# Optimization experiments

Hardware: AMD Instinct MI355X
Metric: run time of the kernel (lower is better)

The kernel has to match this reference:

```python
import jax, jax.numpy as jnp
import numpy as np

T, B, Y, H, R, L = 256, 1024, 32, 1024, 512, 2  # seq_len, batch, y_dim, h_dim, rnn_dim, n_layers


def setup_inputs() -> dict:
    key = jax.random.key(0)
    ks = jax.random.split(key, 18)
    s = jnp.float32(0.05)

    def w(k, shape):
        return jax.random.normal(k, shape, dtype=jnp.float32) * s

    return {
        "y": jax.random.normal(ks[0], (T, B, Y), dtype=jnp.float32),
        # decoder MLP: Linear(R->H), ReLU, Linear(H->H), ReLU
        "dec_w1": w(ks[1], (H, R)), "dec_b1": jnp.zeros((H,), jnp.float32),
        "dec_w2": w(ks[2], (H, H)), "dec_b2": jnp.zeros((H,), jnp.float32),
        # dec_mean: Linear(H->Y); dec_std: Linear(H->Y) + Softplus
        "mean_w": w(ks[3], (Y, H)), "mean_b": jnp.zeros((Y,), jnp.float32),
        "std_w": w(ks[4], (Y, H)), "std_b": jnp.zeros((Y,), jnp.float32),
        # 2-layer GRU, torch gate order (r, z, n)
        "gru_wih0": w(ks[5], (3 * R, Y)), "gru_whh0": w(ks[6], (3 * R, R)),
        "gru_bih0": jnp.zeros((3 * R,), jnp.float32), "gru_bhh0": jnp.zeros((3 * R,), jnp.float32),
        "gru_wih1": w(ks[7], (3 * R, R)), "gru_whh1": w(ks[8], (3 * R, R)),
        "gru_bih1": jnp.zeros((3 * R,), jnp.float32), "gru_bhh1": jnp.zeros((3 * R,), jnp.float32),
    }


def _gru_cell(x, h, wih, whh, bih, bhh):
    # torch GRUCell math, gates ordered (r, z, n)
    gi = x @ wih.T + bih          # [B, 3R]
    gh = h @ whh.T + bhh          # [B, 3R]
    ir, iz, inn = jnp.split(gi, 3, axis=-1)
    hr, hz, hn = jnp.split(gh, 3, axis=-1)
    r = jax.nn.sigmoid(ir + hr)
    z = jax.nn.sigmoid(iz + hz)
    n = jnp.tanh(inn + r * hn)
    return (1.0 - z) * n + z * h


def reference(y, dec_w1, dec_b1, dec_w2, dec_b2, mean_w, mean_b, std_w, std_b,
              gru_wih0, gru_whh0, gru_bih0, gru_bhh0,
              gru_wih1, gru_whh1, gru_bih1, gru_bhh1):
    log2pi = jnp.float32(np.log(2.0 * np.pi))
    batch = y.shape[1]
    h0 = jnp.zeros((L, batch, R), dtype=y.dtype)

    def step(carry, y_t):
        h, nll = carry
        # decode from top-layer hidden state (before the GRU update)
        d = jax.nn.relu(h[-1] @ dec_w1.T + dec_b1)
        d = jax.nn.relu(d @ dec_w2.T + dec_b2)
        mean_t = d @ mean_w.T + mean_b
        std_t = jax.nn.softplus(d @ std_w.T + std_b)
        # nll_gauss: 0.5 * sum((x-mu)^2/std^2 + 2*log(std) + log(2*pi))
        nll_t = 0.5 * jnp.sum((y_t - mean_t) ** 2 / (std_t ** 2)
                              + 2.0 * jnp.log(std_t) + log2pi)
        # single GRU step (2 layers)
        h_l0 = _gru_cell(y_t, h[0], gru_wih0, gru_whh0, gru_bih0, gru_bhh0)
        h_l1 = _gru_cell(h_l0, h[1], gru_wih1, gru_whh1, gru_bih1, gru_bhh1)
        return (jnp.stack([h_l0, h_l1]), nll + nll_t), None

    (_, nll), _ = jax.lax.scan(step, (h0, jnp.float32(0.0)), y)
    return nll
```

## Files before the change

kernel.cpp:

```cpp
#include <hip/hip_runtime.h>
#include <math.h>

#define TT   256
#define BB   1024
#define YDIM 32
#define HDIM 1024
#define RDIM 512

typedef __attribute__((ext_vector_type(8))) short frag8;
typedef __attribute__((ext_vector_type(4))) float f32x4;

#define LDS_BUF 16384

#define OFF_NLL   ((size_t)0)
#define OFF_HAF   ((size_t)4096)
#define SZ_HF     ((size_t)BB*RDIM*4)
#define OFF_HBF   (OFF_HAF + 2*SZ_HF)
#define OFF_HA16  (OFF_HBF + 2*SZ_HF)
#define SZ_H16    ((size_t)BB*RDIM*2)
#define OFF_HB16  (OFF_HA16 + 2*SZ_H16)
#define OFF_D1    (OFF_HB16 + 2*SZ_H16)
#define SZ_DBUF   ((size_t)BB*HDIM*2)
#define OFF_D2    (OFF_D1 + 2*SZ_DBUF)
#define OFF_Y16   (OFF_D2 + 2*SZ_DBUF)
#define OFF_WG0I  (OFF_Y16 + (size_t)TT*BB*YDIM*2)
#define OFF_WG0H  (OFF_WG0I + (size_t)1536*YDIM*2)
#define OFF_WG1I  (OFF_WG0H + (size_t)1536*RDIM*2)
#define OFF_WG1H  (OFF_WG1I + (size_t)1536*RDIM*2)
#define OFF_WD1   (OFF_WG1H + (size_t)1536*RDIM*2)
#define OFF_WD2   (OFF_WD1 + (size_t)HDIM*RDIM*2)
#define OFF_WMS   (OFF_WD2 + (size_t)HDIM*HDIM*2)
#define OFF_BI0   (OFF_WMS + (size_t)64*HDIM*2)
#define OFF_BH0   (OFF_BI0 + 1536*4)
#define OFF_BI1   (OFF_BH0 + 1536*4)
#define OFF_BH1   (OFF_BI1 + 1536*4)

__device__ __forceinline__ short f2bf(float f) {
  union { float f; unsigned u; } v; v.f = f;
  unsigned r = (v.u + 0x7fffu + ((v.u >> 16) & 1u)) >> 16;
  return (short)r;
}
__device__ __forceinline__ void cvt8(const float* s, short* d) {
  float4 a = *(const float4*)s;
  float4 b = *(const float4*)(s + 4);
  frag8 v;
  v[0]=f2bf(a.x); v[1]=f2bf(a.y); v[2]=f2bf(a.z); v[3]=f2bf(a.w);
  v[4]=f2bf(b.x); v[5]=f2bf(b.y); v[6]=f2bf(b.z); v[7]=f2bf(b.w);
  *(frag8*)d = v;
}
__device__ __forceinline__ int permRow(int n) {
  int q = n / 48, r = n - 48 * q, g = r >> 4, u = r & 15;
  return g * 512 + q * 16 + u;
}
__device__ __forceinline__ float sigf(float x) { return 1.0f / (1.0f + expf(-x)); }

__device__ __forceinline__ void gload16(const short* g, short* l) {
  __builtin_amdgcn_global_load_lds(
      (const __attribute__((address_space(1))) void*)g,
      (__attribute__((address_space(3))) void*)l, 16, 0, 0);
}

template<int MF, int NF>
__device__ __forceinline__ void kloop64(
    const short* __restrict__ A, int lda, int m0,
    const short* __restrict__ B, int ldb, int nrowsB, int K,
    int wm, int wn, short* lds, f32x4 (*acc)[NF], int tid)
{
  const int l = tid & 63, w = tid >> 6, u = l & 15, quad = l >> 4;
  const int nk = K >> 6;
  const int bunits = nrowsB << 3;

  auto stage = [&](int kc, int buf) {
    short* base = lds + buf * LDS_BUF;
    const int k0 = kc << 6;
    for (int c = (w << 6); c < 1024; c += 256) {
      int p = c + l, r = p >> 3, q = (p & 7) ^ (r & 7);
      gload16(A + (size_t)(m0 + r) * lda + k0 + (q << 3), base + (c << 3));
    }
    short* bb = base + 8192;
    for (int c = (w << 6); c < bunits; c += 256) {
      int p = c + l, r = p >> 3, q = (p & 7) ^ (r & 7);
      gload16(B + (size_t)r * ldb + k0 + (q << 3), bb + (c << 3));
    }
  };

  stage(0, 0);
  __syncthreads();
  for (int kc = 0; kc < nk; ++kc) {
    if (kc + 1 < nk) stage(kc + 1, (kc + 1) & 1);
    const short* base = lds + (kc & 1) * LDS_BUF;
#pragma unroll
    for (int kk2 = 0; kk2 < 2; ++kk2) {
      const int q = (kk2 << 2) + quad;
      const int aoff = (q ^ (u & 7)) << 3;
      frag8 a[MF], b[NF];
#pragma unroll
      for (int i = 0; i < MF; ++i)
        a[i] = *(const frag8*)(base + ((wm + (i << 4) + u) << 6) + aoff);
#pragma unroll
      for (int f = 0; f < NF; ++f)
        b[f] = *(const frag8*)(base + 8192 + ((wn + (f << 4) + u) << 6) + aoff);
#pragma unroll
      for (int i = 0; i < MF; ++i)
#pragma unroll
        for (int f = 0; f < NF; ++f)
          acc[i][f] = __builtin_amdgcn_mfma_f32_16x16x32_bf16(a[i], b[f], acc[i][f], 0, 0, 0);
    }
    __syncthreads();
  }
}

template<int MF, int NF>
__device__ __forceinline__ void kloop32(
    const short* __restrict__ A, int lda, int m0,
    const short* __restrict__ B, int nrowsB,
    int wm, int wn, short* lds, f32x4 (*acc)[NF], int tid)
{
  const int l = tid & 63, w = tid >> 6, u = l & 15, quad = l >> 4;
  short* base = lds;
  for (int c = (w << 6); c < 512; c += 256) {
    int p = c + l, r = p >> 2, q = (p & 3) ^ (r & 3);
    gload16(A + (size_t)(m0 + r) * lda + (q << 3), base + (c << 3));
  }
  short* bb = base + 4096;
  const int bunits = nrowsB << 2;
  for (int c = (w << 6); c < bunits; c += 256) {
    int p = c + l, r = p >> 2, q = (p & 3) ^ (r & 3);
    gload16(B + (size_t)r * 32 + (q << 3), bb + (c << 3));
  }
  __syncthreads();
  const int aoff = (quad ^ (u & 3)) << 3;
  frag8 a[MF], b[NF];
#pragma unroll
  for (int i = 0; i < MF; ++i)
    a[i] = *(const frag8*)(base + ((wm + (i << 4) + u) << 5) + aoff);
#pragma unroll
  for (int f = 0; f < NF; ++f)
    b[f] = *(const frag8*)(base + 4096 + ((wn + (f << 4) + u) << 5) + aoff);
#pragma unroll
  for (int i = 0; i < MF; ++i)
#pragma unroll
    for (int f = 0; f < NF; ++f)
      acc[i][f] = __builtin_amdgcn_mfma_f32_16x16x32_bf16(a[i], b[f], acc[i][f], 0, 0, 0);
  __syncthreads();
}

template<bool GI32>
__device__ void gru_tile(int mb, int nb,
                         const short* Ax, int ldx, const short* Wgi,
                         const short* Ah, const short* Wgh,
                         const float* bi, const float* bh,
                         const float* hold, float* hout, short* h16out,
                         short* lds, int tid)
{
  f32x4 zero = {0.f, 0.f, 0.f, 0.f};
  f32x4 gi[4][3], gh[4][3];
#pragma unroll
  for (int i = 0; i < 4; ++i)
#pragma unroll
    for (int f = 0; f < 3; ++f) { gi[i][f] = zero; gh[i][f] = zero; }
  const int w = tid >> 6, l = tid & 63, u = l & 15, quad = l >> 4;
  const int wm = (w & 1) * 64, wn = (w >> 1) * 48;
  if (GI32)
    kloop32<4, 3>(Ax, ldx, mb * 128, Wgi, 96, wm, wn, lds, gi, tid);
  else
    kloop64<4, 3>(Ax, ldx, mb * 128, Wgi, RDIM, 96, RDIM, wm, wn, lds, gi, tid);
  kloop64<4, 3>(Ah, RDIM, mb * 128, Wgh, RDIM, 96, RDIM, wm, wn, lds, gh, tid);

  const int np = nb * 96 + (w >> 1) * 48 + u;
  const float bir = bi[np], biz = bi[np + 16], bin = bi[np + 32];
  const float bhr = bh[np], bhz = bh[np + 16], bhn = bh[np + 32];
  const int unit = nb * 32 + (w >> 1) * 16 + u;
#pragma unroll
  for (int i = 0; i < 4; ++i)
#pragma unroll
    for (int j = 0; j < 4; ++j) {
      int row = mb * 128 + wm + 16 * i + quad * 4 + j;
      float r = sigf((gi[i][0][j] + bir) + (gh[i][0][j] + bhr));
      float z = sigf((gi[i][1][j] + biz) + (gh[i][1][j] + bhz));
      float n = tanhf((gi[i][2][j] + bin) + r * (gh[i][2][j] + bhn));
      float ho = hold[(size_t)row * RDIM + unit];
      float hn = (1.f - z) * n + z * ho;
      hout[(size_t)row * RDIM + unit] = hn;
      h16out[(size_t)row * RDIM + unit] = f2bf(hn);
    }
}

__device__ void dec_tile(int mb, int nb, const short* A, int lda, int K,
                         const short* W, const float* bias, short* outp,
                         short* lds, int tid)
{
  f32x4 zero = {0.f, 0.f, 0.f, 0.f};
  f32x4 acc[4][4];
#pragma unroll
  for (int i = 0; i < 4; ++i)
#pragma unroll
    for (int f = 0; f < 4; ++f) acc[i][f] = zero;
  const int w = tid >> 6, l = tid & 63, u = l & 15, quad = l >> 4;
  const int wm = (w & 1) * 64, wn = (w >> 1) * 64;
  kloop64<4, 4>(A, lda, mb * 128, W, K, 128, K, wm, wn, lds, acc, tid);
  const int colb = nb * 128 + wn + u;
  float bv[4];
#pragma unroll
  for (int f = 0; f < 4; ++f) bv[f] = bias[colb + 16 * f];
#pragma unroll
  for (int i = 0; i < 4; ++i)
#pragma unroll
    for (int f = 0; f < 4; ++f)
#pragma unroll
      for (int j = 0; j < 4; ++j) {
        int row = mb * 128 + wm + 16 * i + quad * 4 + j;
        float v = acc[i][f][j] + bv[f];
        if (v < 0.f) v = 0.f;
        outp[(size_t)row * HDIM + colb + 16 * f] = f2bf(v);
      }
}

__device__ void ms_tile(int mb, int tstep, const short* d2p, const short* Wms,
                        const float* mbias, const float* sbias, const float* y,
                        float* nll, short* lds, int tid)
{
  f32x4 zero = {0.f, 0.f, 0.f, 0.f};
  f32x4 acc[2][4];
#pragma unroll
  for (int i = 0; i < 2; ++i)
#pragma unroll
    for (int f = 0; f < 4; ++f) acc[i][f] = zero;
  const int w = tid >> 6, l = tid & 63, u = l & 15, quad = l >> 4;
  kloop64<2, 4>(d2p, HDIM, mb * 128, Wms, HDIM, 64, HDIM, w * 32, 0, lds, acc, tid);
  float lsum = 0.f;
#pragma unroll
  for (int i = 0; i < 2; ++i)
#pragma unroll
    for (int j = 0; j < 4; ++j) {
      int row = mb * 128 + w * 32 + 16 * i + quad * 4 + j;
      const float* yr = y + ((size_t)tstep * BB + row) * YDIM;
#pragma unroll
      for (int f = 0; f < 2; ++f) {
        int c = 16 * f + u;
        float m  = acc[i][f][j] + mbias[c];
        float sp = acc[i][f + 2][j] + sbias[c];
        float sg = (sp > 20.f) ? sp : log1pf(expf(sp));
        float dv = (yr[c] - m) / sg;
        lsum += dv * dv + 2.f * logf(sg) + 1.8378770664093453f;
      }
    }
  lsum *= 0.5f;
#pragma unroll
  for (int o = 32; o; o >>= 1) lsum += __shfl_xor(lsum, o);
  if (l == 0) atomicAdd(nll, lsum);
}

__global__ __launch_bounds__(256) void prepack_kernel(
    const float* y, const float* dw1, const float* dw2,
    const float* mw, const float* sw,
    const float* wih0, const float* whh0, const float* bih0, const float* bhh0,
    const float* wih1, const float* whh1, const float* bih1, const float* bhh1,
    char* __restrict__ ws)
{
  const size_t g = (size_t)blockIdx.x * 256 + threadIdx.x;
  const size_t N = (size_t)gridDim.x * 256;
  float4 z4 = {0.f, 0.f, 0.f, 0.f};
  float4* hz = (float4*)(ws + OFF_HAF);
  for (size_t i = g; i < (size_t)4 * BB * RDIM / 4; i += N) hz[i] = z4;
  int4 zi = {0, 0, 0, 0};
  int4* h16z = (int4*)(ws + OFF_HA16);
  for (size_t i = g; i < (size_t)4 * BB * RDIM / 8; i += N) h16z[i] = zi;
  if (g == 0) *(float*)(ws + OFF_NLL) = 0.f;

  short* y16  = (short*)(ws + OFF_Y16);
  short* Wg0i = (short*)(ws + OFF_WG0I);
  short* Wg0h = (short*)(ws + OFF_WG0H);
  short* Wg1i = (short*)(ws + OFF_WG1I);
  short* Wg1h = (short*)(ws + OFF_WG1H);
  short* Wd1  = (short*)(ws + OFF_WD1);
  short* Wd2  = (short*)(ws + OFF_WD2);
  short* Wms  = (short*)(ws + OFF_WMS);
  float* bi0  = (float*)(ws + OFF_BI0);
  float* bh0  = (float*)(ws + OFF_BH0);
  float* bi1  = (float*)(ws + OFF_BI1);
  float* bh1  = (float*)(ws + OFF_BH1);

  for (size_t s = g; s < (size_t)TT * BB * YDIM / 8; s += N)
    cvt8(y + s * 8, y16 + s * 8);
  for (size_t s = g; s < (size_t)1536 * RDIM / 8; s += N) {
    int row = (int)(s >> 6), seg = (int)(s & 63) << 3;
    int pr = permRow(row);
    cvt8(whh0 + (size_t)pr * RDIM + seg, Wg0h + (size_t)row * RDIM + seg);
    cvt8(wih1 + (size_t)pr * RDIM + seg, Wg1i + (size_t)row * RDIM + seg);
    cvt8(whh1 + (size_t)pr * RDIM + seg, Wg1h + (size_t)row * RDIM + seg);
  }
  for (size_t s = g; s < (size_t)1536 * YDIM / 8; s += N) {
    int row = (int)(s >> 2), seg = (int)(s & 3) << 3;
    cvt8(wih0 + (size_t)permRow(row) * YDIM + seg, Wg0i + (size_t)row * YDIM + seg);
  }
  for (size_t s = g; s < (size_t)HDIM * RDIM / 8; s += N)
    cvt8(dw1 + s * 8, Wd1 + s * 8);
  for (size_t s = g; s < (size_t)HDIM * HDIM / 8; s += N)
    cvt8(dw2 + s * 8, Wd2 + s * 8);
  for (size_t s = g; s < (size_t)64 * HDIM / 8; s += N) {
    int row = (int)(s >> 7), seg = (int)(s & 127) << 3;
    const float* src = (row < 32) ? (mw + (size_t)row * HDIM + seg)
                                  : (sw + (size_t)(row - 32) * HDIM + seg);
    cvt8(src, Wms + (size_t)row * HDIM + seg);
  }
  for (size_t s = g; s < 1536; s += N) {
    int pr = permRow((int)s);
    bi0[s] = bih0[pr]; bh0[s] = bhh0[pr];
    bi1[s] = bih1[pr]; bh1[s] = bhh1[pr];
  }
}

__global__ __launch_bounds__(256, 2) void phase_kernel(
    int p, const float* __restrict__ y,
    const float* db1, const float* db2, const float* mbias, const float* sbias,
    char* __restrict__ ws)
{
  __shared__ short lds[2 * LDS_BUF];
  const int tid = threadIdx.x;
  const int t = blockIdx.x;
  const int cur = p & 1, prv = cur ^ 1;

  float* hAf = (float*)(ws + OFF_HAF);
  float* hBf = (float*)(ws + OFF_HBF);
  short* hA16 = (short*)(ws + OFF_HA16);
  short* hB16 = (short*)(ws + OFF_HB16);
  short* d10 = (short*)(ws + OFF_D1);
  short* d20 = (short*)(ws + OFF_D2);
  const short* y16 = (const short*)(ws + OFF_Y16);

  float* hAfc = hAf + (size_t)cur * BB * RDIM;
  float* hAfp = hAf + (size_t)prv * BB * RDIM;
  float* hBfc = hBf + (size_t)cur * BB * RDIM;
  float* hBfp = hBf + (size_t)prv * BB * RDIM;
  short* hA16c = hA16 + (size_t)cur * BB * RDIM;
  short* hA16p = hA16 + (size_t)prv * BB * RDIM;
  short* hB16c = hB16 + (size_t)cur * BB * RDIM;
  short* hB16p = hB16 + (size_t)prv * BB * RDIM;
  short* d1c = d10 + (size_t)cur * BB * HDIM;
  short* d1p = d10 + (size_t)prv * BB * HDIM;
  short* d2c = d20 + (size_t)cur * BB * HDIM;
  short* d2p = d20 + (size_t)prv * BB * HDIM;

  const short* Wg0i = (const short*)(ws + OFF_WG0I);
  const short* Wg0h = (const short*)(ws + OFF_WG0H);
  const short* Wg1i = (const short*)(ws + OFF_WG1I);
  const short* Wg1h = (const short*)(ws + OFF_WG1H);
  const short* Wd1  = (const short*)(ws + OFF_WD1);
  const short* Wd2  = (const short*)(ws + OFF_WD2);
  const short* Wms  = (const short*)(ws + OFF_WMS);
  const float* bi0  = (const float*)(ws + OFF_BI0);
  const float* bh0  = (const float*)(ws + OFF_BH0);
  const float* bi1  = (const float*)(ws + OFF_BI1);
  const float* bh1  = (const float*)(ws + OFF_BH1);
  float* nllp = (float*)(ws + OFF_NLL);

  if (t < 128) {
    if (p >= 1 && p <= 255) {
      int mb = t >> 4, nb = t & 15;
      gru_tile<false>(mb, nb,
                      hA16p, RDIM, Wg1i + (size_t)nb * 96 * RDIM,
                      hB16p, Wg1h + (size_t)nb * 96 * RDIM,
                      bi1, bh1, hBfp, hBfc, hB16c, lds, tid);
    }
  } else if (t < 192) {
    if (p >= 2 && p <= 257) {
      int q = t - 128, mb = q >> 3, nb = q & 7;
      dec_tile(mb, nb, d1p, HDIM, HDIM, Wd2 + (size_t)nb * 128 * HDIM,
               db2, d2c, lds, tid);
    }
  } else if (t < 200) {
    if (p >= 3 && p <= 258) {
      ms_tile(t - 192, p - 3, d2p, Wms, mbias, sbias, y, nllp, lds, tid);
    }
  } else if (t < 328) {
    if (p <= 255) {
      int q = t - 200, mb = q >> 4, nb = q & 15;
      gru_tile<true>(mb, nb,
                     y16 + (size_t)p * BB * YDIM, YDIM, Wg0i + (size_t)nb * 96 * YDIM,
                     hA16p, Wg0h + (size_t)nb * 96 * RDIM,
                     bi0, bh0, hAfp, hAfc, hA16c, lds, tid);
    }
  } else {
    if (p >= 1 && p <= 256) {
      int q = t - 328, mb = q >> 3, nb = q & 7;
      dec_tile(mb, nb, hB16p, RDIM, RDIM, Wd1 + (size_t)nb * 128 * RDIM,
               db1, d1c, lds, tid);
    }
  }
}

__global__ void finish_kernel(float* out, const char* ws)
{
  if (threadIdx.x == 0 && blockIdx.x == 0)
    out[0] = *(const float*)(ws + OFF_NLL);
}

extern "C" void kernel_launch(void* const* d_in, const int* in_sizes, int n_in,
                              void* d_out, int out_size, void* d_ws, size_t ws_size,
                              hipStream_t stream) {
  (void)in_sizes; (void)n_in; (void)out_size; (void)ws_size;
  const float* y    = (const float*)d_in[0];
  const float* dw1  = (const float*)d_in[1];
  const float* db1  = (const float*)d_in[2];
  const float* dw2  = (const float*)d_in[3];
  const float* db2  = (const float*)d_in[4];
  const float* mw   = (const float*)d_in[5];
  const float* mbias= (const float*)d_in[6];
  const float* sw   = (const float*)d_in[7];
  const float* sbias= (const float*)d_in[8];
  const float* wih0 = (const float*)d_in[9];
  const float* whh0 = (const float*)d_in[10];
  const float* bih0 = (const float*)d_in[11];
  const float* bhh0 = (const float*)d_in[12];
  const float* wih1 = (const float*)d_in[13];
  const float* whh1 = (const float*)d_in[14];
  const float* bih1 = (const float*)d_in[15];
  const float* bhh1 = (const float*)d_in[16];
  char* ws = (char*)d_ws;
  float* out = (float*)d_out;

  prepack_kernel<<<256, 256, 0, stream>>>(y, dw1, dw2, mw, sw,
                                          wih0, whh0, bih0, bhh0,
                                          wih1, whh1, bih1, bhh1, ws);
  for (int p = 0; p < 259; ++p)
    phase_kernel<<<392, 256, 0, stream>>>(p, y, db1, db2, mbias, sbias, ws);
  finish_kernel<<<1, 1, 0, stream>>>(out, ws);
}
```

Before: 5.804 ms.

## Widen GRU tiles, fuse gi/gh accumulation, use K=32 double-buffered loops

GRU tiles now cover 192 gate columns (64 hidden units) instead of 96. The input and hidden GEMMs accumulate into a shared accumulator for the r and z gates, with a separate slot for the hidden n part. All K-loops switch from 64-wide to 32-wide chunks with smaller double buffers, and LDS shrinks to 40KB. The grid drops from 392 to 264 blocks, which should roughly halve the A-operand reloads per GRU. The trade-off is fewer blocks for parallelism and more register pressure, since the accumulator grows from 24 to 32 f32x4.

Measured after the change: 9.601 ms. +65.4%, slower.

```diff
diff --git a/kernel.cpp b/kernel.cpp
--- a/kernel.cpp
+++ b/kernel.cpp
@@ -9,8 +9,6 @@
 
 typedef __attribute__((ext_vector_type(8))) short frag8;
 typedef __attribute__((ext_vector_type(4))) float f32x4;
-
-#define LDS_BUF 16384
 
 #define OFF_NLL   ((size_t)0)
 #define OFF_HAF   ((size_t)4096)
@@ -60,130 +58,148 @@
       (__attribute__((address_space(3))) void*)l, 16, 0, 0);
 }
 
-template<int MF, int NF>
-__device__ __forceinline__ void kloop64(
+template<int AROWS, int BROWS, int MF, int NF>
+__device__ __forceinline__ void kloop32(
     const short* __restrict__ A, int lda, int m0,
-    const short* __restrict__ B, int ldb, int nrowsB, int K,
+    const short* __restrict__ B, int ldb, int K,
     int wm, int wn, short* lds, f32x4 (*acc)[NF], int tid)
 {
+  constexpr int BSTR = (AROWS + BROWS) * 32;
   const int l = tid & 63, w = tid >> 6, u = l & 15, quad = l >> 4;
-  const int nk = K >> 6;
-  const int bunits = nrowsB << 3;
-
-  auto stage = [&](int kc, int buf) {
-    short* base = lds + buf * LDS_BUF;
-    const int k0 = kc << 6;
-    for (int c = (w << 6); c < 1024; c += 256) {
-      int p = c + l, r = p >> 3, q = (p & 7) ^ (r & 7);
-      gload16(A + (size_t)(m0 + r) * lda + k0 + (q << 3), base + (c << 3));
-    }
-    short* bb = base + 8192;
-    for (int c = (w << 6); c < bunits; c += 256) {
-      int p = c + l, r = p >> 3, q = (p & 7) ^ (r & 7);
+  const int nk = K >> 5;
+
+  auto stage = [&](int kc, short* buf) {
+    const int k0 = kc << 5;
+    for (int c = (w << 6); c < AROWS * 4; c += 256) {
+      int p = c + l, r = p >> 2, q = (p & 3) ^ (r & 3);
+      gload16(A + (size_t)(m0 + r) * lda + k0 + (q << 3), buf + (c << 3));
+    }
+    short* bb = buf + AROWS * 32;
+    for (int c = (w << 6); c < BROWS * 4; c += 256) {
+      int p = c + l, r = p >> 2, q = (p & 3) ^ (r & 3);
       gload16(B + (size_t)r * ldb + k0 + (q << 3), bb + (c << 3));
     }
   };
 
-  stage(0, 0);
+  stage(0, lds);
   __syncthreads();
   for (int kc = 0; kc < nk; ++kc) {
-    if (kc + 1 < nk) stage(kc + 1, (kc + 1) & 1);
-    const short* base = lds + (kc & 1) * LDS_BUF;
-#pragma unroll
-    for (int kk2 = 0; kk2 < 2; ++kk2) {
-      const int q = (kk2 << 2) + quad;
-      const int aoff = (q ^ (u & 7)) << 3;
-      frag8 a[MF], b[NF];
-#pragma unroll
-      for (int i = 0; i < MF; ++i)
-        a[i] = *(const frag8*)(base + ((wm + (i << 4) + u) << 6) + aoff);
+    if (kc + 1 < nk) stage(kc + 1, lds + ((kc + 1) & 1) * BSTR);
+    const short* base = lds + (kc & 1) * BSTR;
+    const int ao = (quad ^ (u & 3)) << 3;
+    frag8 a[MF], b[NF];
+#pragma unroll
+    for (int i = 0; i < MF; ++i)
+      a[i] = *(const frag8*)(base + (wm + (i << 4) + u) * 32 + ao);
+#pragma unroll
+    for (int f = 0; f < NF; ++f)
+      b[f] = *(const frag8*)(base + AROWS * 32 + (wn + (f << 4) + u) * 32 + ao);
+#pragma unroll
+    for (int i = 0; i < MF; ++i)
 #pragma unroll
       for (int f = 0; f < NF; ++f)
-        b[f] = *(const frag8*)(base + 8192 + ((wn + (f << 4) + u) << 6) + aoff);
-#pragma unroll
-      for (int i = 0; i < MF; ++i)
-#pragma unroll
-        for (int f = 0; f < NF; ++f)
-          acc[i][f] = __builtin_amdgcn_mfma_f32_16x16x32_bf16(a[i], b[f], acc[i][f], 0, 0, 0);
-    }
+        acc[i][f] = __builtin_amdgcn_mfma_f32_16x16x32_bf16(a[i], b[f], acc[i][f], 0, 0, 0);
     __syncthreads();
   }
 }
 
-template<int MF, int NF>
-__device__ __forceinline__ void kloop32(
+template<int NSEL>
+__device__ __forceinline__ void kloop_gru(
     const short* __restrict__ A, int lda, int m0,
-    const short* __restrict__ B, int nrowsB,
-    int wm, int wn, short* lds, f32x4 (*acc)[NF], int tid)
-{
+    const short* __restrict__ B, int ldb, int K,
+    short* lds, f32x4 (*acc)[2][4], int tid)
+{
+  constexpr int BSTR = (128 + 192) * 32;
   const int l = tid & 63, w = tid >> 6, u = l & 15, quad = l >> 4;
-  short* base = lds;
-  for (int c = (w << 6); c < 512; c += 256) {
-    int p = c + l, r = p >> 2, q = (p & 3) ^ (r & 3);
-    gload16(A + (size_t)(m0 + r) * lda + (q << 3), base + (c << 3));
-  }
-  short* bb = base + 4096;
-  const int bunits = nrowsB << 2;
-  for (int c = (w << 6); c < bunits; c += 256) {
-    int p = c + l, r = p >> 2, q = (p & 3) ^ (r & 3);
-    gload16(B + (size_t)r * 32 + (q << 3), bb + (c << 3));
-  }
+  const int nk = K >> 5;
+  const int wm = (w & 1) * 64;
+  const int glb = (w >> 1) * 2;
+
+  auto stage = [&](int kc, short* buf) {
+    const int k0 = kc << 5;
+    for (int c = (w << 6); c < 512; c += 256) {
+      int p = c + l, r = p >> 2, q = (p & 3) ^ (r & 3);
+      gload16(A + (size_t)(m0 + r) * lda + k0 + (q << 3), buf + (c << 3));
+    }
+    short* bb = buf + 4096;
+    for (int c = (w << 6); c < 768; c += 256) {
+      int p = c + l, r = p >> 2, q = (p & 3) ^ (r & 3);
+      gload16(B + (size_t)r * ldb + k0 + (q << 3), bb + (c << 3));
+    }
+  };
+
+  stage(0, lds);
   __syncthreads();
-  const int aoff = (quad ^ (u & 3)) << 3;
-  frag8 a[MF], b[NF];
-#pragma unroll
-  for (int i = 0; i < MF; ++i)
-    a[i] = *(const frag8*)(base + ((wm + (i << 4) + u) << 5) + aoff);
-#pragma unroll
-  for (int f = 0; f < NF; ++f)
-    b[f] = *(const frag8*)(base + 4096 + ((wn + (f << 4) + u) << 5) + aoff);
-#pragma unroll
-  for (int i = 0; i < MF; ++i)
-#pragma unroll
-    for (int f = 0; f < NF; ++f)
-      acc[i][f] = __builtin_amdgcn_mfma_f32_16x16x32_bf16(a[i], b[f], acc[i][f], 0, 0, 0);
-  __syncthreads();
-}
-
-template<bool GI32>
-__device__ void gru_tile(int mb, int nb,
-                         const short* Ax, int ldx, const short* Wgi,
-                         const short* Ah, const short* Wgh,
-                         const float* bi, const float* bh,
-                         const float* hold, float* hout, short* h16out,
-                         short* lds, int tid)
-{
+  for (int kc = 0; kc < nk; ++kc) {
+    if (kc + 1 < nk) stage(kc + 1, lds + ((kc + 1) & 1) * BSTR);
+    const short* base = lds + (kc & 1) * BSTR;
+    const short* bb = base + 4096;
+    const int ao = (quad ^ (u & 3)) << 3;
+    frag8 a[4], b[2][3];
+#pragma unroll
+    for (int i = 0; i < 4; ++i)
+      a[i] = *(const frag8*)(base + (wm + (i << 4) + u) * 32 + ao);
+#pragma unroll
+    for (int g = 0; g < 2; ++g)
+#pragma unroll
+      for (int f = 0; f < 3; ++f)
+        b[g][f] = *(const frag8*)(bb + (((glb + g) * 48 + f * 16 + u) * 32) + ao);
+#pragma unroll
+    for (int i = 0; i < 4; ++i)
+#pragma unroll
+      for (int g = 0; g < 2; ++g) {
+        acc[i][g][0]    = __builtin_amdgcn_mfma_f32_16x16x32_bf16(a[i], b[g][0], acc[i][g][0], 0, 0, 0);
+        acc[i][g][1]    = __builtin_amdgcn_mfma_f32_16x16x32_bf16(a[i], b[g][1], acc[i][g][1], 0, 0, 0);
+        acc[i][g][NSEL] = __builtin_amdgcn_mfma_f32_16x16x32_bf16(a[i], b[g][2], acc[i][g][NSEL], 0, 0, 0);
+      }
+    __syncthreads();
+  }
+}
+
+__device__ void gru5(int mb, int nb,
+    const short* Ax, int ldax, int Kx,
+    const short* Ah,
+    const short* Wgi, int ldwi,
+    const short* Wgh,
+    const float* bi, const float* bh,
+    const float* hold, float* hout, short* h16out,
+    short* lds, int tid)
+{
+  const int w = tid >> 6, l = tid & 63, u = l & 15, quad = l >> 4;
+  const int wm = (w & 1) * 64;
   f32x4 zero = {0.f, 0.f, 0.f, 0.f};
-  f32x4 gi[4][3], gh[4][3];
+  f32x4 acc[4][2][4];
 #pragma unroll
   for (int i = 0; i < 4; ++i)
 #pragma unroll
-    for (int f = 0; f < 3; ++f) { gi[i][f] = zero; gh[i][f] = zero; }
-  const int w = tid >> 6, l = tid & 63, u = l & 15, quad = l >> 4;
-  const int wm = (w & 1) * 64, wn = (w >> 1) * 48;
-  if (GI32)
-    kloop32<4, 3>(Ax, ldx, mb * 128, Wgi, 96, wm, wn, lds, gi, tid);
-  else
-    kloop64<4, 3>(Ax, ldx, mb * 128, Wgi, RDIM, 96, RDIM, wm, wn, lds, gi, tid);
-  kloop64<4, 3>(Ah, RDIM, mb * 128, Wgh, RDIM, 96, RDIM, wm, wn, lds, gh, tid);
-
-  const int np = nb * 96 + (w >> 1) * 48 + u;
-  const float bir = bi[np], biz = bi[np + 16], bin = bi[np + 32];
-  const float bhr = bh[np], bhz = bh[np + 16], bhn = bh[np + 32];
-  const int unit = nb * 32 + (w >> 1) * 16 + u;
-#pragma unroll
-  for (int i = 0; i < 4; ++i)
-#pragma unroll
-    for (int j = 0; j < 4; ++j) {
-      int row = mb * 128 + wm + 16 * i + quad * 4 + j;
-      float r = sigf((gi[i][0][j] + bir) + (gh[i][0][j] + bhr));
-      float z = sigf((gi[i][1][j] + biz) + (gh[i][1][j] + bhz));
-      float n = tanhf((gi[i][2][j] + bin) + r * (gh[i][2][j] + bhn));
-      float ho = hold[(size_t)row * RDIM + unit];
-      float hn = (1.f - z) * n + z * ho;
-      hout[(size_t)row * RDIM + unit] = hn;
-      h16out[(size_t)row * RDIM + unit] = f2bf(hn);
-    }
+    for (int g = 0; g < 2; ++g)
+#pragma unroll
+      for (int c = 0; c < 4; ++c) acc[i][g][c] = zero;
+
+  kloop_gru<2>(Ax, ldax, mb * 128, Wgi, ldwi, Kx, lds, acc, tid);
+  kloop_gru<3>(Ah, RDIM, mb * 128, Wgh, RDIM, RDIM, lds, acc, tid);
+
+#pragma unroll
+  for (int g = 0; g < 2; ++g) {
+    const int gl = (w >> 1) * 2 + g;
+    const int npg = nb * 192 + gl * 48 + u;
+    const float bir = bi[npg], biz = bi[npg + 16], bin = bi[npg + 32];
+    const float bhr = bh[npg], bhz = bh[npg + 16], bhn = bh[npg + 32];
+    const int unit = nb * 64 + gl * 16 + u;
+#pragma unroll
+    for (int i = 0; i < 4; ++i)
+#pragma unroll
+      for (int j = 0; j < 4; ++j) {
+        int row = mb * 128 + wm + 16 * i + quad * 4 + j;
+        float rr = sigf((acc[i][g][0][j] + bir) + bhr);
+        float zz = sigf((acc[i][g][1][j] + biz) + bhz);
+        float nn = tanhf((acc[i][g][2][j] + bin) + rr * (acc[i][g][3][j] + bhn));
+        float ho = hold[(size_t)row * RDIM + unit];
+        float hv = (1.f - zz) * nn + zz * ho;
+        hout[(size_t)row * RDIM + unit] = hv;
+        h16out[(size_t)row * RDIM + unit] = f2bf(hv);
+      }
+  }
 }
 
 __device__ void dec_tile(int mb, int nb, const short* A, int lda, int K,
@@ -198,7 +214,7 @@
     for (int f = 0; f < 4; ++f) acc[i][f] = zero;
   const int w = tid >> 6, l = tid & 63, u = l & 15, quad = l >> 4;
   const int wm = (w & 1) * 64, wn = (w >> 1) * 64;
-  kloop64<4, 4>(A, lda, mb * 128, W, K, 128, K, wm, wn, lds, acc, tid);
+  kloop32<128, 128, 4, 4>(A, lda, mb * 128, W, K, K, wm, wn, lds, acc, tid);
   const int colb = nb * 128 + wn + u;
   float bv[4];
 #pragma unroll
@@ -227,7 +243,7 @@
 #pragma unroll
     for (int f = 0; f < 4; ++f) acc[i][f] = zero;
   const int w = tid >> 6, l = tid & 63, u = l & 15, quad = l >> 4;
-  kloop64<2, 4>(d2p, HDIM, mb * 128, Wms, HDIM, 64, HDIM, w * 32, 0, lds, acc, tid);
+  kloop32<128, 64, 2, 4>(d2p, HDIM, mb * 128, Wms, HDIM, HDIM, w * 32, 0, lds, acc, tid);
   float lsum = 0.f;
 #pragma unroll
   for (int i = 0; i < 2; ++i)
@@ -283,6 +299,7 @@
 
   for (size_t s = g; s < (size_t)TT * BB * YDIM / 8; s += N)
     cvt8(y + s * 8, y16 + s * 8);
+
   for (size_t s = g; s < (size_t)1536 * RDIM / 8; s += N) {
     int row = (int)(s >> 6), seg = (int)(s & 63) << 3;
     int pr = permRow(row);
@@ -316,7 +333,7 @@
     const float* db1, const float* db2, const float* mbias, const float* sbias,
     char* __restrict__ ws)
 {
-  __shared__ short lds[2 * LDS_BUF];
+  __shared__ short lds[20480];
   const int tid = threadIdx.x;
   const int t = blockIdx.x;
   const int cur = p & 1, prv = cur ^ 1;
@@ -355,37 +372,41 @@
   const float* bh1  = (const float*)(ws + OFF_BH1);
   float* nllp = (float*)(ws + OFF_NLL);
 
-  if (t < 128) {
+  if (t < 64) {
     if (p >= 1 && p <= 255) {
-      int mb = t >> 4, nb = t & 15;
-      gru_tile<false>(mb, nb,
-                      hA16p, RDIM, Wg1i + (size_t)nb * 96 * RDIM,
-                      hB16p, Wg1h + (size_t)nb * 96 * RDIM,
-                      bi1, bh1, hBfp, hBfc, hB16c, lds, tid);
+      int mb = t >> 3, nb = t & 7;
+      gru5(mb, nb,
+           hA16p, RDIM, RDIM,
+           hB16p,
+           Wg1i + (size_t)nb * 192 * RDIM, RDIM,
+           Wg1h + (size_t)nb * 192 * RDIM,
+           bi1, bh1, hBfp, hBfc, hB16c, lds, tid);
+    }
+  } else if (t < 128) {
+    if (p <= 255) {
+      int q = t - 64, mb = q >> 3, nb = q & 7;
+      gru5(mb, nb,
+           y16 + (size_t)p * BB * YDIM, YDIM, YDIM,
+           hA16p,
+           Wg0i + (size_t)nb * 192 * YDIM, YDIM,
+           Wg0h + (size_t)nb * 192 * RDIM,
+           bi0, bh0, hAfp, hAfc, hA16c, lds, tid);
     }
   } else if (t < 192) {
+    if (p >= 1 && p <= 256) {
+      int q = t - 128, mb = q >> 3, nb = q & 7;
+      dec_tile(mb, nb, hB16p, RDIM, RDIM, Wd1 + (size_t)nb * 128 * RDIM,
+               db1, d1c, lds, tid);
+    }
+  } else if (t < 256) {
     if (p >= 2 && p <= 257) {
-      int q = t - 128, mb = q >> 3, nb = q & 7;
+      int q = t - 192, mb = q >> 3, nb = q & 7;
       dec_tile(mb, nb, d1p, HDIM, HDIM, Wd2 + (size_t)nb * 128 * HDIM,
                db2, d2c, lds, tid);
     }
-  } else if (t < 200) {
+  } else {
     if (p >= 3 && p <= 258) {
-      ms_tile(t - 192, p - 3, d2p, Wms, mbias, sbias, y, nllp, lds, tid);
-    }
-  } else if (t < 328) {
-    if (p <= 255) {
-      int q = t - 200, mb = q >> 4, nb = q & 15;
-      gru_tile<true>(mb, nb,
-                     y16 + (size_t)p * BB * YDIM, YDIM, Wg0i + (size_t)nb * 96 * YDIM,
-                     hA16p, Wg0h + (size_t)nb * 96 * RDIM,
-                     bi0, bh0, hAfp, hAfc, hA16c, lds, tid);
-    }
-  } else {
-    if (p >= 1 && p <= 256) {
-      int q = t - 328, mb = q >> 3, nb = q & 7;
-      dec_tile(mb, nb, hB16p, RDIM, RDIM, Wd1 + (size_t)nb * 128 * RDIM,
-               db1, d1c, lds, tid);
+      ms_tile(t - 256, p - 3, d2p, Wms, mbias, sbias, y, nllp, lds, tid);
     }
   }
 }
@@ -424,6 +445,6 @@
                                           wih0, whh0, bih0, bhh0,
                                           wih1, whh1, bih1, bhh1, ws);
   for (int p = 0; p < 259; ++p)
-    phase_kernel<<<392, 256, 0, stream>>>(p, y, db1, db2, mbias, sbias, ws);
+    phase_kernel<<<264, 256, 0, stream>>>(p, y, db1, db2, mbias, sbias, ws);
   finish_kernel<<<1, 1, 0, stream>>>(out, ws);
 }
```
